# Optimization experiments

Hardware: AMD Instinct MI355X
Metric: run time of the kernel (lower is better)

The kernel has to match this reference:

```python
import jax, jax.numpy as jnp
import numpy as np


def _mlp(x, params):
    # params: list of (W, b); tanh on all layers except the last (linear head)
    h = x
    n = len(params)
    for i, (W, b) in enumerate(params):
        h = h @ W + b
        if i < n - 1:
            h = jnp.tanh(h)
    return h


def setup_inputs() -> dict:
    key = jax.random.key(0)
    D, H, B = 32, 256, 2048
    ks = jax.random.split(key, 13)

    def init_w(k, fan_in, fan_out):
        return jax.random.normal(k, (fan_in, fan_out), dtype=jnp.float32) / np.sqrt(fan_in)

    inp = {"x": jax.random.normal(ks[0], (B, D), dtype=jnp.float32)}
    # score net: D -> H -> H -> D
    inp["sW1"] = init_w(ks[1], D, H); inp["sb1"] = jnp.zeros((H,), jnp.float32)
    inp["sW2"] = init_w(ks[2], H, H); inp["sb2"] = jnp.zeros((H,), jnp.float32)
    inp["sW3"] = init_w(ks[3], H, D); inp["sb3"] = jnp.zeros((D,), jnp.float32)
    # covariance net: D -> H -> H -> D*D
    inp["cW1"] = init_w(ks[4], D, H); inp["cb1"] = jnp.zeros((H,), jnp.float32)
    inp["cW2"] = init_w(ks[5], H, H); inp["cb2"] = jnp.zeros((H,), jnp.float32)
    inp["cW3"] = init_w(ks[6], H, D * D); inp["cb3"] = jnp.zeros((D * D,), jnp.float32)
    return inp


def reference(x, sW1, sb1, sW2, sb2, sW3, sb3, cW1, cb1, cW2, cb2, cW3, cb3):
    B = x.shape[0]
    d = sW1.shape[0]
    sp = [(sW1, sb1), (sW2, sb2), (sW3, sb3)]
    cp = [(cW1, cb1), (cW2, cb2), (cW3, cb3)]

    # score and trace of its Jacobian (hutchinson_samples == 0 path)
    score = _mlp(x, sp)                                   # [B, d]
    score_fn = lambda xi: _mlp(xi, sp)
    Js = jax.vmap(jax.jacfwd(score_fn))(x)                # [B, d, d]
    jacobian_trace = jnp.trace(Js, axis1=1, axis2=2)      # [B]

    # covariance net and its divergence: cov_div[b, i] = sum_j d cov[b, i, j] / d x[b, j]
    cov = _mlp(x, cp).reshape(B, d, d)                    # [B, d, d]
    cov_fn = lambda xi: _mlp(xi, cp)
    Jc = jax.vmap(jax.jacfwd(cov_fn))(x).reshape(B, d, d, d)  # [B, i, j, j_in]
    cov_div = jnp.einsum('bijj->bi', Jc)                  # [B, d]

    return (score, jacobian_trace, cov, cov_div)
```

## Files before the change

### kernel.cpp

```cpp
#include <hip/hip_runtime.h>
#include <math.h>

#define Dd 32
#define Hh 256

using short8   = __attribute__((ext_vector_type(8))) short;
using floatx4  = __attribute__((ext_vector_type(4))) float;
typedef unsigned short ushort4v __attribute__((ext_vector_type(4)));

__device__ inline unsigned short f2bf(float f) {
    union { float f; unsigned u; } v; v.f = f;
    unsigned r = (v.u + 0x7FFFu + ((v.u >> 16) & 1u)) >> 16;
    return (unsigned short)r;
}
__device__ inline float bf2f(unsigned short h) {
    union { unsigned u; float f; } v; v.u = ((unsigned)h) << 16;
    return v.f;
}
__device__ inline float fast_tanh(float z) {
    float e = __expf(2.0f * z);
    return 1.0f - 2.0f * __builtin_amdgcn_rcpf(e + 1.0f);
}

__device__ inline size_t offFrag256(int row, int k) {
    return ((size_t)((row >> 4) * 8 + (k >> 5))) * 512
         + (((k & 31) >> 3) * 16 + (row & 15)) * 8 + (k & 7);
}

__global__ __launch_bounds__(256) void k1_prep(
    const float* __restrict__ sW1, const float* __restrict__ sW2, const float* __restrict__ sW3,
    const float* __restrict__ cW1, const float* __restrict__ cW2, const float* __restrict__ cW3,
    unsigned short* __restrict__ cW3t,
    unsigned short* __restrict__ sW2t, unsigned short* __restrict__ cW2t,
    unsigned short* __restrict__ sW3t,
    unsigned short* __restrict__ W1ts, unsigned short* __restrict__ W1tc)
{
    __shared__ float fl[64][33];
    const int tid = threadIdx.x;
    const int bid = blockIdx.x;

    if (bid < 49) {
        const float* src; unsigned short* dst; int stride, n0;
        if (bid < 32)      { src = cW3; dst = cW3t; stride = 1024; n0 = bid * 32; }
        else if (bid < 40) { src = sW2; dst = sW2t; stride = 256;  n0 = (bid - 32) * 32; }
        else if (bid < 48) { src = cW2; dst = cW2t; stride = 256;  n0 = (bid - 40) * 32; }
        else               { src = sW3; dst = sW3t; stride = 32;   n0 = 0; }

        const int nn  = tid & 31, kg = tid >> 5;
        const int nn2 = tid >> 3, ks = (tid & 7) * 8;

        for (int p = 0; p < 4; ++p) {
            if (p) __syncthreads();
            #pragma unroll
            for (int j = 0; j < 8; ++j) {
                int kk = kg * 8 + j;
                fl[kk][nn] = src[(size_t)(p * 64 + kk) * stride + n0 + nn];
            }
            __syncthreads();
            short8 v;
            #pragma unroll
            for (int j = 0; j < 8; ++j) v[j] = (short)f2bf(fl[ks + j][nn2]);
            *(short8*)(dst + offFrag256(n0 + nn2, p * 64 + ks)) = v;
        }
        return;
    }
    {
        const float* W1 = (bid == 49) ? sW1 : cW1;
        unsigned short* dst = (bid == 49) ? W1ts : W1tc;
        const int n = tid;
        #pragma unroll
        for (int c8 = 0; c8 < 4; ++c8) {
            short8 v;
            #pragma unroll
            for (int j = 0; j < 8; ++j)
                v[j] = (short)f2bf(W1[(size_t)(c8 * 8 + j) * 256 + n]);
            *(short8*)(dst + (size_t)(n >> 4) * 512 + (c8 * 16 + (n & 15)) * 8) = v;
        }
    }
}

__global__ __launch_bounds__(512, 2) void ka_mfma(
    const float* __restrict__ x,
    const float* __restrict__ sW1, const float* __restrict__ sW2, const float* __restrict__ sW3,
    const float* __restrict__ cW1, const float* __restrict__ cW2, const float* __restrict__ cW3,
    const unsigned short* __restrict__ W1ts, const unsigned short* __restrict__ W1tc,
    const unsigned short* __restrict__ sW2t, const unsigned short* __restrict__ cW2t,
    const unsigned short* __restrict__ sW3t,
    const float* __restrict__ sb1, const float* __restrict__ sb2, const float* __restrict__ sb3,
    const float* __restrict__ cb1, const float* __restrict__ cb2,
    float* __restrict__ out_score,
    unsigned short* __restrict__ T1s, unsigned short* __restrict__ T2s,
    unsigned short* __restrict__ T1c, unsigned short* __restrict__ T2c,
    unsigned short* __restrict__ H2c, unsigned short* __restrict__ Mt)
{
    __shared__ char smem[43008];
    const int tid = threadIdx.x;
    const int bid = blockIdx.x;

    if (bid >= 256) {
        const int pb = bid - 256;
        const int kq = pb & 3;
        const int i  = pb >> 2;
        float (*W1t)[36] = (float(*)[36])smem;
        float (*ctS)[33] = (float(*)[33])(smem + 9216);

        const float *W1, *W2, *C3;
        int cstride, coff;
        if (i == 0) { W1 = sW1; W2 = sW2; C3 = sW3; cstride = 32;   coff = 0; }
        else        { W1 = cW1; W2 = cW2; C3 = cW3; cstride = 1024; coff = (i - 1) * 32; }

        {
            int kl = tid & 63, jg = tid >> 6;
            #pragma unroll
            for (int jj = 0; jj < 4; ++jj) {
                int j = jg * 4 + jj;
                W1t[kl][j] = W1[j * 256 + kq * 64 + kl];
            }
        }
        {
            const int row0 = tid >> 5, col = tid & 31;
            #pragma unroll
            for (int p8 = 0; p8 < 16; ++p8) {
                int row = p8 * 16 + row0;
                ctS[row][col] = C3[(size_t)row * cstride + coff + col];
            }
        }
        __syncthreads();

        const int t     = tid & 255;
        const int khalf = tid >> 8;
        float ct[32];
        #pragma unroll
        for (int j = 0; j < 32; ++j) ct[j] = ctS[t][j];

        for (int kg = khalf * 4; kg < khalf * 4 + 4; ++kg) {
            const int kbase = kq * 64 + kg * 8;
            short8 pk;
            #pragma unroll
            for (int q = 0; q < 8; ++q) {
                float a = 0.f;
                #pragma unroll
                for (int j4 = 0; j4 < 8; ++j4) {
                    float4 w = *(const float4*)&W1t[kg * 8 + q][j4 * 4];
                    a += w.x * ct[j4 * 4 + 0] + w.y * ct[j4 * 4 + 1]
                       + w.z * ct[j4 * 4 + 2] + w.w * ct[j4 * 4 + 3];
                }
                float m = a * W2[(size_t)(kbase + q) * 256 + t];
                pk[q] = (short)f2bf(m);
            }
            *(short8*)(Mt + (size_t)i * 65536 + offFrag256(t, kbase)) = pk;
        }
        return;
    }

    const int net = bid & 1;
    const int sb  = (bid >> 1) * 16;

    const unsigned short* W1t = net ? W1tc : W1ts;
    const unsigned short* W2t = net ? cW2t : sW2t;
    const float* b1 = net ? cb1 : sb1;
    const float* b2 = net ? cb2 : sb2;
    unsigned short* T1 = net ? T1c : T1s;
    unsigned short* T2 = net ? T2c : T2s;

    unsigned short (*hB)[264] = (unsigned short(*)[264])smem;

    const int w    = tid >> 6;
    const int lane = tid & 63;
    const int g    = lane >> 4;
    const int r16  = lane & 15;

    short8 ax;
    {
        const float* xs = x + (size_t)(sb + r16) * 32 + g * 8;
        float4 a = *(const float4*)xs;
        float4 b = *(const float4*)(xs + 4);
        ax[0] = (short)f2bf(a.x); ax[1] = (short)f2bf(a.y);
        ax[2] = (short)f2bf(a.z); ax[3] = (short)f2bf(a.w);
        ax[4] = (short)f2bf(b.x); ax[5] = (short)f2bf(b.y);
        ax[6] = (short)f2bf(b.z); ax[7] = (short)f2bf(b.w);
    }

    #pragma unroll
    for (int nt = 0; nt < 2; ++nt) {
        const int ti = w * 2 + nt;
        const int nb = ti * 16;
        short8 bf = *(const short8*)(W1t + (size_t)ti * 512 + lane * 8);
        floatx4 acc = (floatx4){0.f, 0.f, 0.f, 0.f};
        acc = __builtin_amdgcn_mfma_f32_16x16x32_bf16(ax, bf, acc, 0, 0, 0);
        const float bias = b1[nb + r16];
        #pragma unroll
        for (int reg = 0; reg < 4; ++reg) {
            float h = fast_tanh(acc[reg] + bias);
            int m = g * 4 + reg;
            int k = nb + r16;
            hB[m][k] = f2bf(h);
            T1[(size_t)(sb >> 4) * 4096 + offFrag256(m, k)] = f2bf(1.0f - h * h);
        }
    }
    __syncthreads();

    short8 bfr[8];
    #pragma unroll
    for (int ks = 0; ks < 8; ++ks)
        bfr[ks] = *(const short8*)&hB[r16][ks * 32 + g * 8];

    const int stile64 = sb >> 6;
    const int mt64    = (sb >> 4) & 3;

    unsigned short h2st[2][4];
    #pragma unroll
    for (int mt = 0; mt < 2; ++mt) {
        const int ti = w * 2 + mt;
        const int cb = ti * 16;
        floatx4 acc = (floatx4){0.f, 0.f, 0.f, 0.f};
        #pragma unroll
        for (int ks = 0; ks < 8; ++ks) {
            short8 af = *(const short8*)(W2t + (size_t)(ti * 8 + ks) * 512 + lane * 8);
            acc = __builtin_amdgcn_mfma_f32_16x16x32_bf16(af, bfr[ks], acc, 0, 0, 0);
        }
        #pragma unroll
        for (int reg = 0; reg < 4; ++reg) {
            const int c2 = cb + g * 4 + reg;
            float h = fast_tanh(acc[reg] + b2[c2]);
            unsigned short hb = f2bf(h);
            T2[(size_t)stile64 * 16384
               + (size_t)(mt64 * 16 + (c2 >> 4)) * 256
               + ((c2 & 15) + (r16 >> 2) * 16) * 4 + (r16 & 3)] = f2bf(1.0f - h * h);
            if (net)
                H2c[(size_t)(sb >> 4) * 4096 + offFrag256(r16, c2)] = hb;
            h2st[mt][reg] = hb;
        }
    }

    if (!net) {
        __syncthreads();
        #pragma unroll
        for (int mt = 0; mt < 2; ++mt)
            #pragma unroll
            for (int reg = 0; reg < 4; ++reg)
                hB[r16][(w * 2 + mt) * 16 + g * 4 + reg] = h2st[mt][reg];
        __syncthreads();

        if (w < 2) {
            floatx4 acc = (floatx4){0.f, 0.f, 0.f, 0.f};
            #pragma unroll
            for (int ks = 0; ks < 8; ++ks) {
                short8 af = *(const short8*)(sW3t + (size_t)(w * 8 + ks) * 512 + lane * 8);
                short8 bf = *(const short8*)&hB[r16][ks * 32 + g * 8];
                acc = __builtin_amdgcn_mfma_f32_16x16x32_bf16(af, bf, acc, 0, 0, 0);
            }
            #pragma unroll
            for (int reg = 0; reg < 4; ++reg) {
                const int m = w * 16 + g * 4 + reg;
                out_score[(size_t)(sb + r16) * 32 + m] = acc[reg] + sb3[m];
            }
        }
    }
}

__global__ __launch_bounds__(256, 3) void kb_mfma(
    const unsigned short* __restrict__ T1s, const unsigned short* __restrict__ T2s,
    const unsigned short* __restrict__ T1c, const unsigned short* __restrict__ T2c,
    const unsigned short* __restrict__ H2c,
    const unsigned short* __restrict__ Mt,  const unsigned short* __restrict__ cW3t,
    const float* __restrict__ cb3,
    float* __restrict__ out_trace, float* __restrict__ out_cdiv,
    float* __restrict__ out_cov)
{
    const int stile = blockIdx.x;
    const int job   = blockIdx.y;
    const int sbase = stile * 64;
    const bool contr = (job < 33);

    const unsigned short* A   = contr ? (job == 0 ? T1s : T1c) : H2c;
    const unsigned short* Bm  = contr ? (Mt + (size_t)job * 65536)
                                      : (cW3t + (size_t)(job - 33) * 65536);
    const unsigned short* T2f = (job == 0) ? T2s : T2c;

    __shared__ float red[4][64];

    const int tid  = threadIdx.x;
    const int w    = tid >> 6;
    const int lane = tid & 63;
    const int g    = lane >> 4;
    const int r16  = lane & 15;
    const int st4  = stile * 4;

    floatx4 acc[4][4];
    #pragma unroll
    for (int mt = 0; mt < 4; ++mt)
        #pragma unroll
        for (int nt = 0; nt < 4; ++nt)
            acc[mt][nt] = (floatx4){0.f, 0.f, 0.f, 0.f};

    #pragma unroll
    for (int c = 0; c < 8; ++c) {
        short8 af[4], bf[4];
        #pragma unroll
        for (int mt = 0; mt < 4; ++mt)
            af[mt] = *(const short8*)(A + (size_t)((st4 + mt) * 8 + c) * 512 + lane * 8);
        #pragma unroll
        for (int nt = 0; nt < 4; ++nt)
            bf[nt] = *(const short8*)(Bm + (size_t)((w * 4 + nt) * 8 + c) * 512 + lane * 8);
        #pragma unroll
        for (int mt = 0; mt < 4; ++mt)
            #pragma unroll
            for (int nt = 0; nt < 4; ++nt)
                acc[mt][nt] = __builtin_amdgcn_mfma_f32_16x16x32_bf16(af[mt], bf[nt], acc[mt][nt], 0, 0, 0);
    }

    if (contr) {
        float pp[4][4];
        #pragma unroll
        for (int mt = 0; mt < 4; ++mt)
            #pragma unroll
            for (int reg = 0; reg < 4; ++reg) pp[mt][reg] = 0.f;

        #pragma unroll
        for (int mt = 0; mt < 4; ++mt)
            #pragma unroll
            for (int nt = 0; nt < 4; ++nt) {
                ushort4v t2q = *(const ushort4v*)(T2f + (size_t)stile * 16384
                                 + (size_t)((mt * 16 + (w * 4 + nt)) * 64 + lane) * 4);
                #pragma unroll
                for (int reg = 0; reg < 4; ++reg)
                    pp[mt][reg] += acc[mt][nt][reg] * bf2f(t2q[reg]);
            }

        #pragma unroll
        for (int mt = 0; mt < 4; ++mt)
            #pragma unroll
            for (int reg = 0; reg < 4; ++reg) {
                float v = pp[mt][reg];
                v += __shfl_xor(v, 1, 64);
                v += __shfl_xor(v, 2, 64);
                v += __shfl_xor(v, 4, 64);
                v += __shfl_xor(v, 8, 64);
                pp[mt][reg] = v;
            }
        if (r16 == 0) {
            #pragma unroll
            for (int mt = 0; mt < 4; ++mt)
                #pragma unroll
                for (int reg = 0; reg < 4; ++reg)
                    red[w][mt * 16 + g * 4 + reg] = pp[mt][reg];
        }
        __syncthreads();
        if (tid < 64) {
            float v = red[0][tid] + red[1][tid] + red[2][tid] + red[3][tid];
            int sg = sbase + tid;
            if (job == 0) out_trace[sg] = v;
            else          out_cdiv[(size_t)sg * Dd + (job - 1)] = v;
        }
    } else {
        const int n0 = (job - 33) * 256;
        #pragma unroll
        for (int mt = 0; mt < 4; ++mt)
            #pragma unroll
            for (int nt = 0; nt < 4; ++nt) {
                const int n = (w * 4 + nt) * 16 + r16;
                const float bias = cb3[n0 + n];
                #pragma unroll
                for (int reg = 0; reg < 4; ++reg) {
                    const int r = mt * 16 + g * 4 + reg;
                    out_cov[(size_t)(sbase + r) * 1024 + n0 + n] = acc[mt][nt][reg] + bias;
                }
            }
    }
}

extern "C" void kernel_launch(void* const* d_in, const int* in_sizes, int n_in,
                              void* d_out, int out_size, void* d_ws, size_t ws_size,
                              hipStream_t stream) {
    const float* x   = (const float*)d_in[0];
    const float* sW1 = (const float*)d_in[1];
    const float* sb1 = (const float*)d_in[2];
    const float* sW2 = (const float*)d_in[3];
    const float* sb2 = (const float*)d_in[4];
    const float* sW3 = (const float*)d_in[5];
    const float* sb3 = (const float*)d_in[6];
    const float* cW1 = (const float*)d_in[7];
    const float* cb1 = (const float*)d_in[8];
    const float* cW2 = (const float*)d_in[9];
    const float* cb2 = (const float*)d_in[10];
    const float* cW3 = (const float*)d_in[11];
    const float* cb3 = (const float*)d_in[12];

    const int B = in_sizes[0] / Dd;

    float* out       = (float*)d_out;
    float* out_score = out;
    float* out_trace = out + (size_t)B * Dd;
    float* out_cov   = out_trace + B;
    float* out_cdiv  = out_cov + (size_t)B * Dd * Dd;

    unsigned short* ws16 = (unsigned short*)d_ws;
    const size_t SZ = (size_t)B * 256;
    unsigned short* T1s  = ws16;
    unsigned short* T2s  = ws16 + SZ;
    unsigned short* T1c  = ws16 + 2 * SZ;
    unsigned short* T2c  = ws16 + 3 * SZ;
    unsigned short* H2c  = ws16 + 4 * SZ;
    unsigned short* Mt   = ws16 + 5 * SZ;
    unsigned short* cW3t = Mt + (size_t)33 * 65536;
    unsigned short* sW2t = cW3t + (size_t)1024 * 256;
    unsigned short* cW2t = sW2t + (size_t)256 * 256;
    unsigned short* sW3t = cW2t + (size_t)256 * 256;
    unsigned short* W1ts = sW3t + (size_t)32 * 256;
    unsigned short* W1tc = W1ts + (size_t)256 * 32;

    k1_prep<<<dim3(51), dim3(256), 0, stream>>>(
        sW1, sW2, sW3, cW1, cW2, cW3,
        cW3t, sW2t, cW2t, sW3t, W1ts, W1tc);

    ka_mfma<<<dim3(256 + 132), dim3(512), 0, stream>>>(
        x, sW1, sW2, sW3, cW1, cW2, cW3,
        W1ts, W1tc, sW2t, cW2t, sW3t,
        sb1, sb2, sb3, cb1, cb2,
        out_score, T1s, T2s, T1c, T2c, H2c, Mt);

    kb_mfma<<<dim3(B / 64, 37), dim3(256), 0, stream>>>(
        T1s, T2s, T1c, T2c, H2c, Mt, cW3t, cb3,
        out_trace, out_cdiv, out_cov);
}
```

Measured before the change: 114.3 us.

## Process 32 samples per block in ka and make kb a persistent grid-stride loop

In the first kernel, each block now handles two 16-sample tiles, so the W1/W2 fragments it loads are reused across twice as many samples and the grid shrinks from 256 to 128 MLP blocks. The score head now uses four waves to cover both tiles. The second kernel moves from a 2D grid of 32x37 blocks to 608 persistent blocks that loop over a linearised job/stile index, with an extra barrier so the reduction buffer can be reused. The aim is less redundant weight traffic and less launch and tail imbalance, at the cost of higher register pressure in ka and fewer concurrent blocks.

```diff
diff --git a/kernel.cpp b/kernel.cpp
--- a/kernel.cpp
+++ b/kernel.cpp
@@ -97,8 +97,8 @@
     const int tid = threadIdx.x;
     const int bid = blockIdx.x;
 
-    if (bid >= 256) {
-        const int pb = bid - 256;
+    if (bid >= 128) {
+        const int pb = bid - 128;
         const int kq = pb & 3;
         const int i  = pb >> 2;
         float (*W1t)[36] = (float(*)[36])smem;
@@ -154,7 +154,7 @@
     }
 
     const int net = bid & 1;
-    const int sb  = (bid >> 1) * 16;
+    const int sb  = (bid >> 1) * 32;
 
     const unsigned short* W1t = net ? W1tc : W1ts;
     const unsigned short* W2t = net ? cW2t : sW2t;
@@ -170,15 +170,16 @@
     const int g    = lane >> 4;
     const int r16  = lane & 15;
 
-    short8 ax;
-    {
-        const float* xs = x + (size_t)(sb + r16) * 32 + g * 8;
+    short8 ax[2];
+    #pragma unroll
+    for (int st = 0; st < 2; ++st) {
+        const float* xs = x + (size_t)(sb + st * 16 + r16) * 32 + g * 8;
         float4 a = *(const float4*)xs;
         float4 b = *(const float4*)(xs + 4);
-        ax[0] = (short)f2bf(a.x); ax[1] = (short)f2bf(a.y);
-        ax[2] = (short)f2bf(a.z); ax[3] = (short)f2bf(a.w);
-        ax[4] = (short)f2bf(b.x); ax[5] = (short)f2bf(b.y);
-        ax[6] = (short)f2bf(b.z); ax[7] = (short)f2bf(b.w);
+        ax[st][0] = (short)f2bf(a.x); ax[st][1] = (short)f2bf(a.y);
+        ax[st][2] = (short)f2bf(a.z); ax[st][3] = (short)f2bf(a.w);
+        ax[st][4] = (short)f2bf(b.x); ax[st][5] = (short)f2bf(b.y);
+        ax[st][6] = (short)f2bf(b.z); ax[st][7] = (short)f2bf(b.w);
     }
 
     #pragma unroll
@@ -186,50 +187,61 @@
         const int ti = w * 2 + nt;
         const int nb = ti * 16;
         short8 bf = *(const short8*)(W1t + (size_t)ti * 512 + lane * 8);
-        floatx4 acc = (floatx4){0.f, 0.f, 0.f, 0.f};
-        acc = __builtin_amdgcn_mfma_f32_16x16x32_bf16(ax, bf, acc, 0, 0, 0);
         const float bias = b1[nb + r16];
         #pragma unroll
-        for (int reg = 0; reg < 4; ++reg) {
-            float h = fast_tanh(acc[reg] + bias);
-            int m = g * 4 + reg;
-            int k = nb + r16;
-            hB[m][k] = f2bf(h);
-            T1[(size_t)(sb >> 4) * 4096 + offFrag256(m, k)] = f2bf(1.0f - h * h);
+        for (int st = 0; st < 2; ++st) {
+            floatx4 acc = (floatx4){0.f, 0.f, 0.f, 0.f};
+            acc = __builtin_amdgcn_mfma_f32_16x16x32_bf16(ax[st], bf, acc, 0, 0, 0);
+            #pragma unroll
+            for (int reg = 0; reg < 4; ++reg) {
+                float h = fast_tanh(acc[reg] + bias);
+                int m = g * 4 + reg;
+                int k = nb + r16;
+                hB[st * 16 + m][k] = f2bf(h);
+                T1[(size_t)((sb >> 4) + st) * 4096 + offFrag256(m, k)] = f2bf(1.0f - h * h);
+            }
         }
     }
     __syncthreads();
 
-    short8 bfr[8];
+    short8 bfr[2][8];
     #pragma unroll
-    for (int ks = 0; ks < 8; ++ks)
-        bfr[ks] = *(const short8*)&hB[r16][ks * 32 + g * 8];
-
-    const int stile64 = sb >> 6;
-    const int mt64    = (sb >> 4) & 3;
-
-    unsigned short h2st[2][4];
+    for (int st = 0; st < 2; ++st)
+        #pragma unroll
+        for (int ks = 0; ks < 8; ++ks)
+            bfr[st][ks] = *(const short8*)&hB[st * 16 + r16][ks * 32 + g * 8];
+
+    unsigned short h2st[2][2][4];
     #pragma unroll
     for (int mt = 0; mt < 2; ++mt) {
         const int ti = w * 2 + mt;
         const int cb = ti * 16;
-        floatx4 acc = (floatx4){0.f, 0.f, 0.f, 0.f};
+        floatx4 acc[2];
+        acc[0] = (floatx4){0.f, 0.f, 0.f, 0.f};
+        acc[1] = (floatx4){0.f, 0.f, 0.f, 0.f};
         #pragma unroll
         for (int ks = 0; ks < 8; ++ks) {
             short8 af = *(const short8*)(W2t + (size_t)(ti * 8 + ks) * 512 + lane * 8);
-            acc = __builtin_amdgcn_mfma_f32_16x16x32_bf16(af, bfr[ks], acc, 0, 0, 0);
-        }
-        #pragma unroll
-        for (int reg = 0; reg < 4; ++reg) {
-            const int c2 = cb + g * 4 + reg;
-            float h = fast_tanh(acc[reg] + b2[c2]);
-            unsigned short hb = f2bf(h);
-            T2[(size_t)stile64 * 16384
-               + (size_t)(mt64 * 16 + (c2 >> 4)) * 256
-               + ((c2 & 15) + (r16 >> 2) * 16) * 4 + (r16 & 3)] = f2bf(1.0f - h * h);
-            if (net)
-                H2c[(size_t)(sb >> 4) * 4096 + offFrag256(r16, c2)] = hb;
-            h2st[mt][reg] = hb;
+            acc[0] = __builtin_amdgcn_mfma_f32_16x16x32_bf16(af, bfr[0][ks], acc[0], 0, 0, 0);
+            acc[1] = __builtin_amdgcn_mfma_f32_16x16x32_bf16(af, bfr[1][ks], acc[1], 0, 0, 0);
+        }
+        #pragma unroll
+        for (int st = 0; st < 2; ++st) {
+            const int sg16 = (sb >> 4) + st;
+            const int stile64 = sg16 >> 2;
+            const int mt64    = sg16 & 3;
+            #pragma unroll
+            for (int reg = 0; reg < 4; ++reg) {
+                const int c2 = cb + g * 4 + reg;
+                float h = fast_tanh(acc[st][reg] + b2[c2]);
+                unsigned short hb = f2bf(h);
+                T2[(size_t)stile64 * 16384
+                   + (size_t)(mt64 * 16 + (c2 >> 4)) * 256
+                   + ((c2 & 15) + (r16 >> 2) * 16) * 4 + (r16 & 3)] = f2bf(1.0f - h * h);
+                if (net)
+                    H2c[(size_t)sg16 * 4096 + offFrag256(r16, c2)] = hb;
+                h2st[mt][st][reg] = hb;
+            }
         }
     }
 
@@ -238,22 +250,25 @@
         #pragma unroll
         for (int mt = 0; mt < 2; ++mt)
             #pragma unroll
-            for (int reg = 0; reg < 4; ++reg)
-                hB[r16][(w * 2 + mt) * 16 + g * 4 + reg] = h2st[mt][reg];
+            for (int st = 0; st < 2; ++st)
+                #pragma unroll
+                for (int reg = 0; reg < 4; ++reg)
+                    hB[st * 16 + r16][(w * 2 + mt) * 16 + g * 4 + reg] = h2st[mt][st][reg];
         __syncthreads();
 
-        if (w < 2) {
+        if (w < 4) {
+            const int mtile = w & 1, stile = w >> 1;
             floatx4 acc = (floatx4){0.f, 0.f, 0.f, 0.f};
             #pragma unroll
             for (int ks = 0; ks < 8; ++ks) {
-                short8 af = *(const short8*)(sW3t + (size_t)(w * 8 + ks) * 512 + lane * 8);
-                short8 bf = *(const short8*)&hB[r16][ks * 32 + g * 8];
+                short8 af = *(const short8*)(sW3t + (size_t)(mtile * 8 + ks) * 512 + lane * 8);
+                short8 bf = *(const short8*)&hB[stile * 16 + r16][ks * 32 + g * 8];
                 acc = __builtin_amdgcn_mfma_f32_16x16x32_bf16(af, bf, acc, 0, 0, 0);
             }
             #pragma unroll
             for (int reg = 0; reg < 4; ++reg) {
-                const int m = w * 16 + g * 4 + reg;
-                out_score[(size_t)(sb + r16) * 32 + m] = acc[reg] + sb3[m];
+                const int m = mtile * 16 + g * 4 + reg;
+                out_score[(size_t)(sb + stile * 16 + r16) * 32 + m] = acc[reg] + sb3[m];
             }
         }
     }
@@ -268,16 +283,6 @@
     float* __restrict__ out_trace, float* __restrict__ out_cdiv,
     float* __restrict__ out_cov)
 {
-    const int stile = blockIdx.x;
-    const int job   = blockIdx.y;
-    const int sbase = stile * 64;
-    const bool contr = (job < 33);
-
-    const unsigned short* A   = contr ? (job == 0 ? T1s : T1c) : H2c;
-    const unsigned short* Bm  = contr ? (Mt + (size_t)job * 65536)
-                                      : (cW3t + (size_t)(job - 33) * 65536);
-    const unsigned short* T2f = (job == 0) ? T2s : T2c;
-
     __shared__ float red[4][64];
 
     const int tid  = threadIdx.x;
@@ -285,88 +290,102 @@
     const int lane = tid & 63;
     const int g    = lane >> 4;
     const int r16  = lane & 15;
-    const int st4  = stile * 4;
-
-    floatx4 acc[4][4];
-    #pragma unroll
-    for (int mt = 0; mt < 4; ++mt)
-        #pragma unroll
-        for (int nt = 0; nt < 4; ++nt)
-            acc[mt][nt] = (floatx4){0.f, 0.f, 0.f, 0.f};
-
-    #pragma unroll
-    for (int c = 0; c < 8; ++c) {
-        short8 af[4], bf[4];
+    const int bid  = blockIdx.x;
+
+    for (int u = bid; u < 1184; u += 608) {
+        const int job   = u >> 5;
+        const int stile = u & 31;
+        const int sbase = stile * 64;
+        const bool contr = (job < 33);
+
+        const unsigned short* A   = contr ? (job == 0 ? T1s : T1c) : H2c;
+        const unsigned short* Bm  = contr ? (Mt + (size_t)job * 65536)
+                                          : (cW3t + (size_t)(job - 33) * 65536);
+        const unsigned short* T2f = (job == 0) ? T2s : T2c;
+        const int st4 = stile * 4;
+
+        floatx4 acc[4][4];
         #pragma unroll
         for (int mt = 0; mt < 4; ++mt)
-            af[mt] = *(const short8*)(A + (size_t)((st4 + mt) * 8 + c) * 512 + lane * 8);
-        #pragma unroll
-        for (int nt = 0; nt < 4; ++nt)
-            bf[nt] = *(const short8*)(Bm + (size_t)((w * 4 + nt) * 8 + c) * 512 + lane * 8);
-        #pragma unroll
-        for (int mt = 0; mt < 4; ++mt)
             #pragma unroll
             for (int nt = 0; nt < 4; ++nt)
-                acc[mt][nt] = __builtin_amdgcn_mfma_f32_16x16x32_bf16(af[mt], bf[nt], acc[mt][nt], 0, 0, 0);
-    }
-
-    if (contr) {
-        float pp[4][4];
-        #pragma unroll
-        for (int mt = 0; mt < 4; ++mt)
-            #pragma unroll
-            for (int reg = 0; reg < 4; ++reg) pp[mt][reg] = 0.f;
-
-        #pragma unroll
-        for (int mt = 0; mt < 4; ++mt)
-            #pragma unroll
-            for (int nt = 0; nt < 4; ++nt) {
-                ushort4v t2q = *(const ushort4v*)(T2f + (size_t)stile * 16384
-                                 + (size_t)((mt * 16 + (w * 4 + nt)) * 64 + lane) * 4);
-                #pragma unroll
-                for (int reg = 0; reg < 4; ++reg)
-                    pp[mt][reg] += acc[mt][nt][reg] * bf2f(t2q[reg]);
-            }
-
-        #pragma unroll
-        for (int mt = 0; mt < 4; ++mt)
-            #pragma unroll
-            for (int reg = 0; reg < 4; ++reg) {
-                float v = pp[mt][reg];
-                v += __shfl_xor(v, 1, 64);
-                v += __shfl_xor(v, 2, 64);
-                v += __shfl_xor(v, 4, 64);
-                v += __shfl_xor(v, 8, 64);
-                pp[mt][reg] = v;
-            }
-        if (r16 == 0) {
-            #pragma unroll
-            for (int mt = 0; mt < 4; ++mt)
-                #pragma unroll
-                for (int reg = 0; reg < 4; ++reg)
-                    red[w][mt * 16 + g * 4 + reg] = pp[mt][reg];
-        }
-        __syncthreads();
-        if (tid < 64) {
-            float v = red[0][tid] + red[1][tid] + red[2][tid] + red[3][tid];
-            int sg = sbase + tid;
-            if (job == 0) out_trace[sg] = v;
-            else          out_cdiv[(size_t)sg * Dd + (job - 1)] = v;
-        }
-    } else {
-        const int n0 = (job - 33) * 256;
-        #pragma unroll
-        for (int mt = 0; mt < 4; ++mt)
-            #pragma unroll
-            for (int nt = 0; nt < 4; ++nt) {
-                const int n = (w * 4 + nt) * 16 + r16;
-                const float bias = cb3[n0 + n];
+                acc[mt][nt] = (floatx4){0.f, 0.f, 0.f, 0.f};
+
+        #pragma unroll
+        for (int c = 0; c < 8; ++c) {
+            short8 af[4], bf[4];
+            #pragma unroll
+            for (int mt = 0; mt < 4; ++mt)
+                af[mt] = *(const short8*)(A + (size_t)((st4 + mt) * 8 + c) * 512 + lane * 8);
+            #pragma unroll
+            for (int nt = 0; nt < 4; ++nt)
+                bf[nt] = *(const short8*)(Bm + (size_t)((w * 4 + nt) * 8 + c) * 512 + lane * 8);
+            #pragma unroll
+            for (int mt = 0; mt < 4; ++mt)
+                #pragma unroll
+                for (int nt = 0; nt < 4; ++nt)
+                    acc[mt][nt] = __builtin_amdgcn_mfma_f32_16x16x32_bf16(af[mt], bf[nt], acc[mt][nt], 0, 0, 0);
+        }
+
+        if (contr) {
+            float pp[4][4];
+            #pragma unroll
+            for (int mt = 0; mt < 4; ++mt)
+                #pragma unroll
+                for (int reg = 0; reg < 4; ++reg) pp[mt][reg] = 0.f;
+
+            #pragma unroll
+            for (int mt = 0; mt < 4; ++mt)
+                #pragma unroll
+                for (int nt = 0; nt < 4; ++nt) {
+                    ushort4v t2q = *(const ushort4v*)(T2f + (size_t)stile * 16384
+                                     + (size_t)((mt * 16 + (w * 4 + nt)) * 64 + lane) * 4);
+                    #pragma unroll
+                    for (int reg = 0; reg < 4; ++reg)
+                        pp[mt][reg] += acc[mt][nt][reg] * bf2f(t2q[reg]);
+                }
+
+            #pragma unroll
+            for (int mt = 0; mt < 4; ++mt)
                 #pragma unroll
                 for (int reg = 0; reg < 4; ++reg) {
-                    const int r = mt * 16 + g * 4 + reg;
-                    out_cov[(size_t)(sbase + r) * 1024 + n0 + n] = acc[mt][nt][reg] + bias;
+                    float v = pp[mt][reg];
+                    v += __shfl_xor(v, 1, 64);
+                    v += __shfl_xor(v, 2, 64);
+                    v += __shfl_xor(v, 4, 64);
+                    v += __shfl_xor(v, 8, 64);
+                    pp[mt][reg] = v;
                 }
-            }
+            if (r16 == 0) {
+                #pragma unroll
+                for (int mt = 0; mt < 4; ++mt)
+                    #pragma unroll
+                    for (int reg = 0; reg < 4; ++reg)
+                        red[w][mt * 16 + g * 4 + reg] = pp[mt][reg];
+            }
+            __syncthreads();
+            if (tid < 64) {
+                float v = red[0][tid] + red[1][tid] + red[2][tid] + red[3][tid];
+                int sg = sbase + tid;
+                if (job == 0) out_trace[sg] = v;
+                else          out_cdiv[(size_t)sg * Dd + (job - 1)] = v;
+            }
+            __syncthreads();
+        } else {
+            const int n0 = (job - 33) * 256;
+            #pragma unroll
+            for (int mt = 0; mt < 4; ++mt)
+                #pragma unroll
+                for (int nt = 0; nt < 4; ++nt) {
+                    const int n = (w * 4 + nt) * 16 + r16;
+                    const float bias = cb3[n0 + n];
+                    #pragma unroll
+                    for (int reg = 0; reg < 4; ++reg) {
+                        const int r = mt * 16 + g * 4 + reg;
+                        out_cov[(size_t)(sbase + r) * 1024 + n0 + n] = acc[mt][nt][reg] + bias;
+                    }
+                }
+        }
     }
 }
 
@@ -414,13 +433,13 @@
         sW1, sW2, sW3, cW1, cW2, cW3,
         cW3t, sW2t, cW2t, sW3t, W1ts, W1tc);
 
-    ka_mfma<<<dim3(256 + 132), dim3(512), 0, stream>>>(
+    ka_mfma<<<dim3(128 + 132), dim3(512), 0, stream>>>(
         x, sW1, sW2, sW3, cW1, cW2, cW3,
         W1ts, W1tc, sW2t, cW2t, sW3t,
         sb1, sb2, sb3, cb1, cb2,
         out_score, T1s, T2s, T1c, T2c, H2c, Mt);
 
-    kb_mfma<<<dim3(B / 64, 37), dim3(256), 0, stream>>>(
+    kb_mfma<<<dim3(608), dim3(256), 0, stream>>>(
         T1s, T2s, T1c, T2c, H2c, Mt, cW3t, cb3,
         out_trace, out_cdiv, out_cov);
 }
```

Result: slower. 122.6 us (+7.3%).
